# Performance work log

Hardware: AMD Instinct MI355X
Metric: run time of the kernel (lower is better)

## Reference

```python
import jax, jax.numpy as jnp
import numpy as np

K = 9            # LCN box-filter size
EPS = 1e-6


def _box_sum(x):
    """9x9 box sum with zero padding 4, separable. x: [N,H,W] -> [N,H,W]."""
    xp = x[:, None]                                  # N,1,H,W
    kh = jnp.ones((1, 1, K, 1), x.dtype)
    kw = jnp.ones((1, 1, 1, K), x.dtype)
    y = jax.lax.conv_general_dilated(xp, kh, (1, 1), [(K // 2, K // 2), (0, 0)])
    y = jax.lax.conv_general_dilated(y, kw, (1, 1), [(0, 0), (K // 2, K // 2)])
    return y[:, 0]


def _lcn(img):
    """Faithful to torch: conv weight is ones(3,3,9,9)/81, i.e. the 'mean' SUMS over
    the 3 input channels of per-pixel 9x9 box means; every output channel is identical.
    So compute channel-sum once, box-filter it, and broadcast back over channels."""
    kk = float(K * K)
    mean_local = _box_sum(img.sum(axis=1)) / kk                 # N,H,W
    mean_sq_local = _box_sum((img * img).sum(axis=1)) / kk      # N,H,W
    std_local = (mean_sq_local - mean_local * mean_local) * kk / (kk - 1.0)
    m = mean_local[:, None]                                     # N,1,H,W (broadcasts over C)
    s = std_local[:, None]
    return (img - m) / (s + EPS), m, s


def _warp(right, disp):
    """Equivalent of affine_grid(identity) + grid -= (disp*2/W, 0) + grid_sample
    (bilinear, zeros padding, align_corners=False). Since the y-coordinate is the
    identity grid, iy == row index exactly, so sampling reduces to 1-D horizontal
    bilinear interpolation at source column ix = j - disp[n,i,j]."""
    N, C, H, W = right.shape
    ix = jnp.arange(W, dtype=right.dtype)[None, None, :] - disp   # N,H,W
    x0 = jnp.floor(ix)
    wx = ix - x0                                                  # frac weight for x1
    x0i = x0.astype(jnp.int32)
    x1i = x0i + 1
    v0 = ((x0i >= 0) & (x0i < W)).astype(right.dtype)             # zeros padding masks
    v1 = ((x1i >= 0) & (x1i < W)).astype(right.dtype)
    i0 = jnp.broadcast_to(jnp.clip(x0i, 0, W - 1)[:, None], right.shape)
    i1 = jnp.broadcast_to(jnp.clip(x1i, 0, W - 1)[:, None], right.shape)
    g0 = jnp.take_along_axis(right, i0, axis=3)                   # N,C,H,W
    g1 = jnp.take_along_axis(right, i1, axis=3)
    return g0 * (v0 * (1.0 - wx))[:, None] + g1 * (v1 * wx)[:, None]


def setup_inputs() -> dict:
    key = jax.random.key(0)
    k1, k2, k3 = jax.random.split(key, 3)
    N, C, H, W = 8, 3, 720, 1280
    left_img = jax.random.uniform(k1, (N, C, H, W), dtype=jnp.float32)
    right_img = jax.random.uniform(k2, (N, C, H, W), dtype=jnp.float32)
    dispmap = jax.random.uniform(k3, (N, H, W), dtype=jnp.float32) * 64.0  # pixels
    return {"left_img": left_img, "right_img": right_img, "dispmap": dispmap}


def reference(left_img, right_img, dispmap):
    recon_img = _warp(right_img, dispmap)
    recon_img_lcn, _, _ = _lcn(recon_img)
    left_img_lcn, _, left_std_local = _lcn(left_img)
    return jnp.abs((left_img_lcn - recon_img_lcn) * left_std_local).mean()
```

## Files before the change

kernel.cpp:

```cpp
#include <hip/hip_runtime.h>

#define NB 8
#define CC 3
#define HH 720
#define WW 1280
#define EPSL 1e-6f
#define HSEG 45
#define NSEG (HH / HSEG)
#define OUTC 56
#define NSTRIP 23
#define NITER (HSEG + 8)
#define NUNIT (NSTRIP * NSEG * NB)
#define NBLK (NUNIT / 4)

__global__ __launch_bounds__(256)
void fused_loss_kernel(const float* __restrict__ left,
                       const float* __restrict__ right,
                       const float* __restrict__ disp,
                       float* __restrict__ out)
{
    const int t    = threadIdx.x;
    const int lane = t & 63;
    const int u    = blockIdx.x * 4 + (t >> 6);
    const int strip = u % NSTRIP;
    const int hseg  = (u / NSTRIP) % NSEG;
    const int n     = u / (NSTRIP * NSEG);
    const int h0 = hseg * HSEG;
    const int gc  = strip * OUTC + lane - 4;
    const int gcc = min(max(gc, 0), WW - 1);
    const bool out_lane = (lane >= 4) && (lane < 4 + OUTC) && (gc < WW);
    const size_t plane = (size_t)HH * WW;
    const float* __restrict__ dispn  = disp  + (size_t)n * plane;
    const float* __restrict__ leftn  = left  + (size_t)n * CC * plane;
    const float* __restrict__ rightn = right + (size_t)n * CC * plane;

    float4 rg1 = make_float4(0.f,0.f,0.f,0.f);
    float4 rg2=rg1, rg3=rg1, rg4=rg1, rg5=rg1, rg6=rg1, rg7=rg1, rg8=rg1;
    float p1l0=0,p1l1=0,p1l2=0,p1r0=0,p1r1=0,p1r2=0;
    float p2l0=0,p2l1=0,p2l2=0,p2r0=0,p2r1=0,p2r2=0;
    float p3l0=0,p3l1=0,p3l2=0,p3r0=0,p3r1=0,p3r2=0;
    float p4l0=0,p4l1=0,p4l2=0,p4r0=0,p4r1=0,p4r2=0;

    const int r0 = h0 - 4;

    int rcl = min(max(r0, 0), HH - 1);
    size_t ro = (size_t)rcl * WW + gcc;
    float dA  = dispn[ro];
    float al0 = leftn[ro], al1 = leftn[plane + ro], al2 = leftn[2*plane + ro];
    rcl = min(max(r0 + 1, 0), HH - 1);
    ro  = (size_t)rcl * WW + gcc;
    float dB  = dispn[ro];
    float bl0 = leftn[ro], bl1 = leftn[plane + ro], bl2 = leftn[2*plane + ro];

    float aw0, aw1, ag00, ag01, ag10, ag11, ag20, ag21;
    {
        float ix  = (float)gc - dA;
        float x0f = floorf(ix), wx = ix - x0f;
        int x0i = (int)x0f, x1i = x0i + 1;
        float v0 = (x0i >= 0 && x0i < WW) ? 1.f : 0.f;
        float v1 = (x1i >= 0 && x1i < WW) ? 1.f : 0.f;
        int i0 = min(max(x0i, 0), WW - 1), i1 = min(max(x1i, 0), WW - 1);
        aw0 = v0 * (1.f - wx); aw1 = v1 * wx;
        size_t rb = (size_t)min(max(r0, 0), HH - 1) * WW;
        ag00 = rightn[rb + i0];           ag01 = rightn[rb + i1];
        ag10 = rightn[plane + rb + i0];   ag11 = rightn[plane + rb + i1];
        ag20 = rightn[2*plane + rb + i0]; ag21 = rightn[2*plane + rb + i1];
    }

    float4 vsum = make_float4(0.f,0.f,0.f,0.f);
    float acc = 0.f;

    for (int iter = 0; iter < NITER; ++iter) {
        const int r = r0 + iter;

        int rcl2 = min(max(r + 2, 0), HH - 1);
        size_t ro2 = (size_t)rcl2 * WW + gcc;
        float dC  = dispn[ro2];
        float cl0 = leftn[ro2], cl1 = leftn[plane + ro2], cl2 = leftn[2*plane + ro2];

        float bw0, bw1, bg00, bg01, bg10, bg11, bg20, bg21;
        {
            float ix  = (float)gc - dB;
            float x0f = floorf(ix), wx = ix - x0f;
            int x0i = (int)x0f, x1i = x0i + 1;
            float v0 = (x0i >= 0 && x0i < WW) ? 1.f : 0.f;
            float v1 = (x1i >= 0 && x1i < WW) ? 1.f : 0.f;
            int i0 = min(max(x0i, 0), WW - 1), i1 = min(max(x1i, 0), WW - 1);
            bw0 = v0 * (1.f - wx); bw1 = v1 * wx;
            size_t rb = (size_t)min(max(r + 1, 0), HH - 1) * WW;
            bg00 = rightn[rb + i0];           bg01 = rightn[rb + i1];
            bg10 = rightn[plane + rb + i0];   bg11 = rightn[plane + rb + i1];
            bg20 = rightn[2*plane + rb + i0]; bg21 = rightn[2*plane + rb + i1];
        }

        float rca = ag00*aw0 + ag01*aw1;
        float rcb = ag10*aw0 + ag11*aw1;
        float rcc = ag20*aw0 + ag21*aw1;
        bool valr = (r >= 0) && (r < HH) && (gc >= 0) && (gc < WW);
        float rx = al0 + al1 + al2;
        float ry = al0*al0 + al1*al1 + al2*al2;
        float rz = rca + rcb + rcc;
        float rw = rca*rca + rcb*rcb + rcc*rcc;
        rx = valr ? rx : 0.f;  ry = valr ? ry : 0.f;
        rz = valr ? rz : 0.f;  rw = valr ? rw : 0.f;

        const int sb = lane - 4;
        float hx = __shfl(rx, sb, 64);
        float hy = __shfl(ry, sb, 64);
        float hz = __shfl(rz, sb, 64);
        float hw = __shfl(rw, sb, 64);
#pragma unroll
        for (int k = 1; k < 9; ++k) {
            hx += __shfl(rx, sb + k, 64);
            hy += __shfl(ry, sb + k, 64);
            hz += __shfl(rz, sb + k, 64);
            hw += __shfl(rw, sb + k, 64);
        }

        vsum.x += hx; vsum.y += hy; vsum.z += hz; vsum.w += hw;

        if (iter >= 8) {
            float ml   = vsum.x * (1.f / 81.f);
            float msl  = vsum.y * (1.f / 81.f);
            float stdl = (msl - ml * ml) * (81.f / 80.f);
            float invl = 1.f / (stdl + EPSL);
            float mr   = vsum.z * (1.f / 81.f);
            float msr  = vsum.w * (1.f / 81.f);
            float stdr = (msr - mr * mr) * (81.f / 80.f);
            float invr = 1.f / (stdr + EPSL);
            if (out_lane) {
                float av, bv;
                av = (p4l0 - ml) * invl; bv = (p4r0 - mr) * invr;
                acc += fabsf((av - bv) * stdl);
                av = (p4l1 - ml) * invl; bv = (p4r1 - mr) * invr;
                acc += fabsf((av - bv) * stdl);
                av = (p4l2 - ml) * invl; bv = (p4r2 - mr) * invr;
                acc += fabsf((av - bv) * stdl);
            }
            vsum.x -= rg8.x; vsum.y -= rg8.y; vsum.z -= rg8.z; vsum.w -= rg8.w;
        }

        rg8 = rg7; rg7 = rg6; rg6 = rg5; rg5 = rg4; rg4 = rg3; rg3 = rg2; rg2 = rg1;
        rg1 = make_float4(hx, hy, hz, hw);
        p4l0=p3l0; p4l1=p3l1; p4l2=p3l2; p4r0=p3r0; p4r1=p3r1; p4r2=p3r2;
        p3l0=p2l0; p3l1=p2l1; p3l2=p2l2; p3r0=p2r0; p3r1=p2r1; p3r2=p2r2;
        p2l0=p1l0; p2l1=p1l1; p2l2=p1l2; p2r0=p1r0; p2r1=p1r1; p2r2=p1r2;
        p1l0=al0;  p1l1=al1;  p1l2=al2;  p1r0=rca;  p1r1=rcb;  p1r2=rcc;

        al0=bl0; al1=bl1; al2=bl2;
        aw0=bw0; aw1=bw1;
        ag00=bg00; ag01=bg01; ag10=bg10; ag11=bg11; ag20=bg20; ag21=bg21;
        dB=dC; bl0=cl0; bl1=cl1; bl2=cl2;
    }

#pragma unroll
    for (int off = 32; off > 0; off >>= 1)
        acc += __shfl_down(acc, off, 64);
    __shared__ float red[4];
    if (lane == 0) red[t >> 6] = acc;
    __syncthreads();
    if (t == 0) {
        float s = red[0] + red[1] + red[2] + red[3];
        const float inv_count = 1.f / ((float)NB * CC * HH * WW);
        atomicAdd(out, s * inv_count);
    }
}

extern "C" void kernel_launch(void* const* d_in, const int* in_sizes, int n_in,
                              void* d_out, int out_size, void* d_ws, size_t ws_size,
                              hipStream_t stream) {
    const float* left  = (const float*)d_in[0];
    const float* right = (const float*)d_in[1];
    const float* disp  = (const float*)d_in[2];
    float* out = (float*)d_out;

    hipMemsetAsync(out, 0, sizeof(float) * out_size, stream);

    hipLaunchKernelGGL(fused_loss_kernel, dim3(NBLK), dim3(256), 0, stream,
                       left, right, disp, out);
}
```

Measured before the change: 234.8 us.

## Use two-stage bpermute box sum, fast reciprocal, unrolled loop and shorter segments

Replaces the 9-tap horizontal shuffle sum with a two-stage 3+3 decomposition built on ds_bpermute, cutting cross-lane operations from 36 to 16 per row. It also switches the divisions to hardware approximate reciprocal, splits and unrolls the row loop to remove the per-iteration branch, and adds an occupancy hint to the launch bounds. The row segment is shortened, which creates more blocks for parallelism but raises the fraction of halo rows that are recomputed and reloaded.

```diff
diff --git a/kernel.cpp b/kernel.cpp
--- a/kernel.cpp
+++ b/kernel.cpp
@@ -5,7 +5,7 @@
 #define HH 720
 #define WW 1280
 #define EPSL 1e-6f
-#define HSEG 45
+#define HSEG 24
 #define NSEG (HH / HSEG)
 #define OUTC 56
 #define NSTRIP 23
@@ -13,7 +13,11 @@
 #define NUNIT (NSTRIP * NSEG * NB)
 #define NBLK (NUNIT / 4)
 
-__global__ __launch_bounds__(256)
+__device__ __forceinline__ float bperm(int addr, float x) {
+    return __int_as_float(__builtin_amdgcn_ds_bpermute(addr, __float_as_int(x)));
+}
+
+__global__ __launch_bounds__(256, 5)
 void fused_loss_kernel(const float* __restrict__ left,
                        const float* __restrict__ right,
                        const float* __restrict__ disp,
@@ -34,6 +38,11 @@
     const float* __restrict__ leftn  = left  + (size_t)n * CC * plane;
     const float* __restrict__ rightn = right + (size_t)n * CC * plane;
 
+    const int a_m1 = ((lane + 63) & 63) << 2;
+    const int a_p1 = ((lane +  1) & 63) << 2;
+    const int a_m3 = ((lane + 61) & 63) << 2;
+    const int a_p3 = ((lane +  3) & 63) << 2;
+
     float4 rg1 = make_float4(0.f,0.f,0.f,0.f);
     float4 rg2=rg1, rg3=rg1, rg4=rg1, rg5=rg1, rg6=rg1, rg7=rg1, rg8=rg1;
     float p1l0=0,p1l1=0,p1l2=0,p1r0=0,p1r1=0,p1r2=0;
@@ -51,6 +60,7 @@
     ro  = (size_t)rcl * WW + gcc;
     float dB  = dispn[ro];
     float bl0 = leftn[ro], bl1 = leftn[plane + ro], bl2 = leftn[2*plane + ro];
+    (void)dA;
 
     float aw0, aw1, ag00, ag01, ag10, ag11, ag20, ag21;
     {
@@ -70,7 +80,7 @@
     float4 vsum = make_float4(0.f,0.f,0.f,0.f);
     float acc = 0.f;
 
-    for (int iter = 0; iter < NITER; ++iter) {
+    auto body = [&](int iter, bool do_out) {
         const int r = r0 + iter;
 
         int rcl2 = min(max(r + 2, 0), HH - 1);
@@ -104,30 +114,26 @@
         rx = valr ? rx : 0.f;  ry = valr ? ry : 0.f;
         rz = valr ? rz : 0.f;  rw = valr ? rw : 0.f;
 
-        const int sb = lane - 4;
-        float hx = __shfl(rx, sb, 64);
-        float hy = __shfl(ry, sb, 64);
-        float hz = __shfl(rz, sb, 64);
-        float hw = __shfl(rw, sb, 64);
-#pragma unroll
-        for (int k = 1; k < 9; ++k) {
-            hx += __shfl(rx, sb + k, 64);
-            hy += __shfl(ry, sb + k, 64);
-            hz += __shfl(rz, sb + k, 64);
-            hw += __shfl(rw, sb + k, 64);
-        }
+        float sx = bperm(a_m1, rx) + rx + bperm(a_p1, rx);
+        float sy = bperm(a_m1, ry) + ry + bperm(a_p1, ry);
+        float sz = bperm(a_m1, rz) + rz + bperm(a_p1, rz);
+        float sw = bperm(a_m1, rw) + rw + bperm(a_p1, rw);
+        float hx = bperm(a_m3, sx) + sx + bperm(a_p3, sx);
+        float hy = bperm(a_m3, sy) + sy + bperm(a_p3, sy);
+        float hz = bperm(a_m3, sz) + sz + bperm(a_p3, sz);
+        float hw = bperm(a_m3, sw) + sw + bperm(a_p3, sw);
 
         vsum.x += hx; vsum.y += hy; vsum.z += hz; vsum.w += hw;
 
-        if (iter >= 8) {
+        if (do_out) {
             float ml   = vsum.x * (1.f / 81.f);
             float msl  = vsum.y * (1.f / 81.f);
             float stdl = (msl - ml * ml) * (81.f / 80.f);
-            float invl = 1.f / (stdl + EPSL);
+            float invl = __builtin_amdgcn_rcpf(stdl + EPSL);
             float mr   = vsum.z * (1.f / 81.f);
             float msr  = vsum.w * (1.f / 81.f);
             float stdr = (msr - mr * mr) * (81.f / 80.f);
-            float invr = 1.f / (stdr + EPSL);
+            float invr = __builtin_amdgcn_rcpf(stdr + EPSL);
             if (out_lane) {
                 float av, bv;
                 av = (p4l0 - ml) * invl; bv = (p4r0 - mr) * invr;
@@ -151,7 +157,12 @@
         aw0=bw0; aw1=bw1;
         ag00=bg00; ag01=bg01; ag10=bg10; ag11=bg11; ag20=bg20; ag21=bg21;
         dB=dC; bl0=cl0; bl1=cl1; bl2=cl2;
-    }
+    };
+
+#pragma unroll
+    for (int it = 0; it < 8; ++it) body(it, false);
+#pragma unroll 8
+    for (int it = 8; it < NITER; ++it) body(it, true);
 
 #pragma unroll
     for (int off = 32; off > 0; off >>= 1)
```

Result: slower. 369.8 us (+57.5%).
